# Kernel tuning notes

Hardware: AMD Instinct MI355X
Metric: run time of the kernel (lower is better)

## Reference

```python
import jax, jax.numpy as jnp
import numpy as np

N_NODES = 50000
N_EDGES = 800000
N_REL = 16
N_GRAPHS = 64
IN_DIM = 128
HID = 128
FC = 256
N_CLASSES = 16


def setup_inputs() -> dict:
    key = jax.random.key(0)
    ks = jax.random.split(key, 16)
    h = jax.random.normal(ks[0], (N_NODES, IN_DIM), dtype=jnp.float32)
    src = jax.random.randint(ks[1], (N_EDGES,), 0, N_NODES, dtype=jnp.int32)
    dst = jax.random.randint(ks[2], (N_EDGES,), 0, N_NODES, dtype=jnp.int32)
    rel_types = jax.random.randint(ks[3], (N_EDGES,), 0, N_REL, dtype=jnp.int32)
    graph_ids = jnp.sort(jax.random.randint(ks[4], (N_NODES,), 0, N_GRAPHS, dtype=jnp.int32))
    s1 = 1.0 / np.sqrt(IN_DIM)
    s2 = 1.0 / np.sqrt(HID)
    # RGCN layer 1: per-relation weights, self-loop weight, bias
    W1 = jax.random.normal(ks[5], (N_REL, IN_DIM, HID), dtype=jnp.float32) * s1
    Ws1 = jax.random.normal(ks[6], (IN_DIM, HID), dtype=jnp.float32) * s1
    b1 = jnp.zeros((HID,), dtype=jnp.float32)
    # RGCN layer 2
    W2 = jax.random.normal(ks[7], (N_REL, HID, HID), dtype=jnp.float32) * s2
    Ws2 = jax.random.normal(ks[8], (HID, HID), dtype=jnp.float32) * s2
    b2 = jnp.zeros((HID,), dtype=jnp.float32)
    # FC layer after mean pooling
    Wfc = jax.random.normal(ks[9], (HID, FC), dtype=jnp.float32) * s2
    bfc = jnp.zeros((FC,), dtype=jnp.float32)
    # classify head
    Wc = jax.random.normal(ks[10], (FC, N_CLASSES), dtype=jnp.float32) * (1.0 / np.sqrt(FC))
    bc = jnp.zeros((N_CLASSES,), dtype=jnp.float32)
    return dict(h=h, src=src, dst=dst, rel_types=rel_types, graph_ids=graph_ids,
                W1=W1, Ws1=Ws1, b1=b1, W2=W2, Ws2=Ws2, b2=b2,
                Wfc=Wfc, bfc=bfc, Wc=Wc, bc=bc)


def _rel_graph_conv(h, W, Ws, b, src, dst, rel):
    # dgl RelGraphConv (regularizer=None, self_loop=True, bias=True):
    # out[v] = sum_{e:(u->v)} W[rel_e] @ h[u] + Ws @ h[v] + b
    hW = jnp.einsum('ni,rio->rno', h, W)            # [R, N, out]
    msg = hW[rel, src]                               # [E, out] gather per edge
    agg = jax.ops.segment_sum(msg, dst, num_segments=N_NODES)
    return agg + h @ Ws + b


def _mean_nodes(h, graph_ids):
    sums = jax.ops.segment_sum(h, graph_ids, num_segments=N_GRAPHS)      # [G, D]
    cnts = jax.ops.segment_sum(jnp.ones((h.shape[0], 1), h.dtype), graph_ids,
                               num_segments=N_GRAPHS)                    # [G, 1]
    return sums / jnp.maximum(cnts, 1.0)


def reference(h, src, dst, rel_types, graph_ids,
              W1, Ws1, b1, W2, Ws2, b2, Wfc, bfc, Wc, bc):
    h = h.astype(jnp.float32)
    h = jax.nn.relu(_rel_graph_conv(h, W1, Ws1, b1, src, dst, rel_types))
    h = jax.nn.relu(_rel_graph_conv(h, W2, Ws2, b2, src, dst, rel_types))
    hg = _mean_nodes(h, graph_ids)                   # [G, HID]
    hg = jax.nn.relu(hg @ Wfc + bfc)                 # [G, FC]
    return jax.nn.softmax(hg @ Wc + bc, axis=1)      # [G, n_classes]
```

## Files before the change

kernel.cpp:

```cpp
#include <hip/hip_runtime.h>
#include <hip/hip_bf16.h>

#define N_NODES   50000
#define N_PAD     50048
#define N_EDGES   800000
#define N_REL     16
#define N_GRAPHS  64
#define DIM       128
#define FC_DIM    256
#define N_CLASSES 16

#define SB        50176
#define NBINS_P   (16 * SB)
#define NBLK_PP   784
#define NCOARSE   782
#define NCH       98
#define CHSZ      8192
#define POOL_CH   64
#define NBVIRT    13328
#define GRID_A    1024

#define NBLK_CX   27200
#define XW_TOTAL  (N_PAD * DIM + 2 * 17 * 16384)

#define WS_MARK   0
#define WS_HG     802816
#define WS_CNT    835584
#define WS_SRCOF  835840
#define MEMSET_SZ 4038912
#define WS_BLKH   4038912
#define WS_COFS   4345600
#define WS_PARTP  4348928
#define WS_BLKB   4352256
#define WS_RELB   4355584
#define WS_CIDMAP 4355840
#define WS_RTMP   7567104
#define WS_RECS   10767104
#define WS_OFFSD  13967104
#define WS_X1     14167552
#define WS_X2     26979840
#define WS_AGG    39792128
#define WS_WB     52604416
#define WS_T      53718528

typedef __attribute__((ext_vector_type(8))) short bf16x8;
typedef __attribute__((ext_vector_type(4))) float f32x4;

__device__ __forceinline__ void atomAddF(float* p, float v) {
#if defined(__gfx90a__) || defined(__gfx942__) || defined(__gfx950__)
    unsafeAtomicAdd(p, v);
#else
    atomicAdd(p, v);
#endif
}

__device__ __forceinline__ float bf2f(unsigned int u) {
    union { float f; unsigned int i; } x; x.i = u << 16; return x.f;
}
__device__ __forceinline__ unsigned short f2bf(float f) {
    union { float f; unsigned int u; } x; x.f = f;
    unsigned int r = x.u + 0x7fff + ((x.u >> 16) & 1);
    return (unsigned short)(r >> 16);
}
__device__ __forceinline__ void accum8(float* qa, uint4 u) {
    qa[0] += bf2f(u.x & 0xffff); qa[1] += bf2f(u.x >> 16);
    qa[2] += bf2f(u.y & 0xffff); qa[3] += bf2f(u.y >> 16);
    qa[4] += bf2f(u.z & 0xffff); qa[5] += bf2f(u.z >> 16);
    qa[6] += bf2f(u.w & 0xffff); qa[7] += bf2f(u.w >> 16);
}
__device__ __forceinline__ void pack16(const float* qa, unsigned short* dst) {
    #pragma unroll
    for (int j = 0; j < 2; ++j) {
        uint4 w;
        w.x = ((unsigned int)f2bf(qa[j*8+1]) << 16) | f2bf(qa[j*8+0]);
        w.y = ((unsigned int)f2bf(qa[j*8+3]) << 16) | f2bf(qa[j*8+2]);
        w.z = ((unsigned int)f2bf(qa[j*8+5]) << 16) | f2bf(qa[j*8+4]);
        w.w = ((unsigned int)f2bf(qa[j*8+7]) << 16) | f2bf(qa[j*8+6]);
        ((uint4*)dst)[j] = w;
    }
}

__global__ __launch_bounds__(256) void k_h1cx(
    const int* __restrict__ src, const int* __restrict__ dst, const int* __restrict__ rel,
    unsigned char* __restrict__ mark, int* __restrict__ blockHist,
    const float* __restrict__ h, unsigned short* __restrict__ x1,
    const float* __restrict__ W1, const float* __restrict__ Ws1,
    const float* __restrict__ W2, const float* __restrict__ Ws2,
    unsigned short* __restrict__ Wb)
{
    __shared__ int hl[NCOARSE];
    int t = threadIdx.x;
    if (blockIdx.x < NCH) {
        int b = blockIdx.x;
        for (int i = t; i < NCOARSE; i += 256) hl[i] = 0;
        __syncthreads();
        int e0 = b * CHSZ;
        int eend = min(e0 + CHSZ, N_EDGES);
        for (int e = e0 + t; e < eend; e += 256) {
            int d = dst[e];
            mark[rel[e] * SB + src[e]] = 1;
            atomicAdd(&hl[d >> 6], 1);
        }
        __syncthreads();
        for (int i = t; i < NCOARSE; i += 256) blockHist[b * NCOARSE + i] = hl[i];
    } else {
        int id = (blockIdx.x - NCH) * 256 + t;
        if (id < N_PAD * DIM) {
            int v = id >> 7;
            x1[id] = (v < N_NODES) ? f2bf(h[id]) : (unsigned short)0;
        } else {
            int tt = id - N_PAD * DIM;
            int l = tt / 278528, rem = tt % 278528;
            int r = rem >> 14, rr = rem & 16383;
            int n = rr >> 7, k = rr & 127;
            const float* W  = l ? W2 : W1;
            const float* Ws = l ? Ws2 : Ws1;
            float v = (r < 16) ? W[r * 16384 + k * 128 + n] : Ws[k * 128 + n];
            Wb[tt] = f2bf(v);
        }
    }
}

__global__ __launch_bounds__(256) void k_sA(
    const unsigned int* __restrict__ markU, int* __restrict__ partP,
    int* __restrict__ blockHist, int* __restrict__ cOffs)
{
    int t = threadIdx.x;
    if (blockIdx.x < NBLK_PP) {
        __shared__ int red[256];
        int b = blockIdx.x;
        unsigned int u = markU[b * 256 + t];
        red[t] = (int)((u & 1) + ((u >> 8) & 1) + ((u >> 16) & 1) + ((u >> 24) & 1));
        __syncthreads();
        for (int o = 128; o > 0; o >>= 1) {
            if (t < o) red[t] += red[t + o];
            __syncthreads();
        }
        if (t == 0) partP[b] = red[0];
    } else {
        __shared__ int sc[2][128];
        int i = blockIdx.x - NBLK_PP;
        int v = 0;
        if (t < NCH) v = blockHist[t * NCOARSE + i];
        if (t < 128) sc[0][t] = v;
        __syncthreads();
        int cur = 0, nxt = 1;
        #pragma unroll
        for (int o = 1; o < 128; o <<= 1) {
            if (t < 128) sc[nxt][t] = sc[cur][t] + ((t >= o) ? sc[cur][t - o] : 0);
            __syncthreads();
            int tmp = cur; cur = nxt; nxt = tmp;
        }
        if (t < NCH) blockHist[t * NCOARSE + i] = sc[cur][t] - v;
        if (t == NCH - 1) cOffs[i] = sc[cur][t];
    }
}

__global__ __launch_bounds__(1024) void k_sB(
    const int* __restrict__ partP, int* __restrict__ blkB, int* __restrict__ relB,
    int* __restrict__ cOffs)
{
    int t = threadIdx.x;
    if (blockIdx.x == 0) {
        __shared__ int s1[784], s2[784];
        __shared__ int tot[16], rbase[17];
        int rel = t / 49, pos = t - rel * 49;
        int v = (t < 784) ? partP[t] : 0;
        if (t < 784) s1[t] = v;
        __syncthreads();
        int* cur = s1; int* nxt = s2;
        for (int o = 1; o < 64; o <<= 1) {
            if (t < 784) nxt[t] = cur[t] + ((pos >= o) ? cur[t - o] : 0);
            __syncthreads();
            int* tmp = cur; cur = nxt; nxt = tmp;
        }
        if (t < 784 && pos == 48) tot[rel] = cur[t];
        __syncthreads();
        if (t == 0) {
            int base = 0;
            for (int r = 0; r < 16; ++r) { rbase[r] = base; base += (tot[r] + 63) & ~63; }
            rbase[16] = base;
        }
        __syncthreads();
        if (t < 784) blkB[t] = rbase[rel] + cur[t] - v;
        if (t < 17)  relB[t] = rbase[t];
    } else {
        __shared__ int c1[1024], c2[1024];
        int v = (t < NCOARSE) ? cOffs[t] : 0;
        c1[t] = v; __syncthreads();
        int* cur = c1; int* nxt = c2;
        for (int o = 1; o < 1024; o <<= 1) {
            nxt[t] = cur[t] + ((t >= o) ? cur[t - o] : 0);
            __syncthreads();
            int* tmp = cur; cur = nxt; nxt = tmp;
        }
        if (t < NCOARSE) cOffs[t] = cur[t] - v;
        if (t == NCOARSE) cOffs[NCOARSE] = cur[NCOARSE - 1];
    }
}

__global__ void k_scanPC(const unsigned int* __restrict__ markU, const int* __restrict__ blkB,
                         int* __restrict__ cidMap, int* __restrict__ srcOf) {
    __shared__ int s1[256], s2[256];
    int b = blockIdx.x, t = threadIdx.x;
    unsigned int u = markU[b * 256 + t];
    int f0 = (int)(u & 1), f1 = (int)((u >> 8) & 1);
    int f2 = (int)((u >> 16) & 1), f3 = (int)((u >> 24) & 1);
    int sum = f0 + f1 + f2 + f3;
    s1[t] = sum; __syncthreads();
    int* cur = s1; int* nxt = s2;
    for (int o = 1; o < 256; o <<= 1) {
        nxt[t] = cur[t] + ((t >= o) ? cur[t - o] : 0);
        __syncthreads();
        int* tmp = cur; cur = nxt; nxt = tmp;
    }
    int cid = blkB[b] + cur[t] - sum;
    int rel = b / 49;
    int key0 = b * 1024 + t * 4;
    int srcBase = key0 - rel * SB;
    if (f0) { cidMap[key0]     = cid; srcOf[cid] = srcBase;     cid++; }
    if (f1) { cidMap[key0 + 1] = cid; srcOf[cid] = srcBase + 1; cid++; }
    if (f2) { cidMap[key0 + 2] = cid; srcOf[cid] = srcBase + 2; cid++; }
    if (f3) { cidMap[key0 + 3] = cid; srcOf[cid] = srcBase + 3; cid++; }
}

__global__ __launch_bounds__(256) void k_scat1(
    const int* __restrict__ src, const int* __restrict__ dst, const int* __restrict__ rel,
    const int* __restrict__ cidMap, const int* __restrict__ blockHist,
    const int* __restrict__ cOffs, unsigned int* __restrict__ rtmp)
{
    __shared__ int baseL[NCOARSE];
    __shared__ int hl[NCOARSE];
    int b = blockIdx.x, t = threadIdx.x;
    for (int i = t; i < NCOARSE; i += 256) {
        baseL[i] = blockHist[b * NCOARSE + i] + cOffs[i];
        hl[i] = 0;
    }
    __syncthreads();
    int e0 = b * CHSZ;
    int eend = min(e0 + CHSZ, N_EDGES);
    for (int e = e0 + t; e < eend; e += 256) {
        int d = dst[e];
        int cid = cidMap[rel[e] * SB + src[e]];
        int c = d >> 6;
        int rank = atomicAdd(&hl[c], 1);
        rtmp[baseL[c] + rank] = ((unsigned int)cid << 6) | (unsigned int)(d & 63);
    }
}

__global__ __launch_bounds__(256) void k_p2(
    const unsigned int* __restrict__ rtmp, const int* __restrict__ coarseOffs,
    unsigned int* __restrict__ recs, int* __restrict__ offsD)
{
    __shared__ int cntL[64], exclL[65], cur2[64];
    int i = blockIdx.x, t = threadIdx.x;
    int segB = coarseOffs[i], segE = coarseOffs[i + 1];
    if (t < 64) { cntL[t] = 0; cur2[t] = 0; }
    __syncthreads();
    for (int e = segB + t; e < segE; e += 256)
        atomicAdd(&cntL[rtmp[e] & 63u], 1);
    __syncthreads();
    if (t == 0) {
        int run = segB;
        #pragma unroll
        for (int d = 0; d < 64; ++d) { exclL[d] = run; run += cntL[d]; }
        exclL[64] = run;
    }
    __syncthreads();
    if (t < 64) offsD[i * 64 + t] = exclL[t];
    if (t == 64) offsD[i * 64 + 64] = exclL[64];
    for (int e = segB + t; e < segE; e += 256) {
        unsigned int r = rtmp[e];
        int d = (int)(r & 63u);
        int rank = atomicAdd(&cur2[d], 1);
        recs[exclL[d] + rank] = r >> 6;
    }
}

__global__ __launch_bounds__(256) void k_phaseA(
    const unsigned short* __restrict__ x, const unsigned short* __restrict__ Wb,
    const int* __restrict__ srcOf, const int* __restrict__ relB,
    unsigned short* __restrict__ T)
{
    __shared__ __attribute__((aligned(16))) unsigned short Xs[64 * 136];
    __shared__ __attribute__((aligned(16))) unsigned short Cs[64 * 136];
    __shared__ int sRB[17];

    int tid = threadIdx.x;
    if (tid < 17) sRB[tid] = relB[tid];
    __syncthreads();
    int rtot = sRB[16];

    int row = tid >> 2, c0 = tid & 3;

    auto tileInfo = [&](int vb, int& trow0, int& tr) -> bool {
        int chunk = vb / 136;
        int lane = vb - chunk * 136;
        int r = lane >> 3;
        int i = chunk * 8 + (lane & 7);
        int base, cnt;
        if (r == 16) { base = rtot; cnt = N_PAD / 64; }
        else         { base = sRB[r]; cnt = (sRB[r + 1] - base) >> 6; }
        if (i >= cnt) return false;
        trow0 = base + i * 64; tr = r;
        return true;
    };

    int vb = blockIdx.x;
    int cur_row0, cur_r;
    while (vb < NBVIRT && !tileInfo(vb, cur_row0, cur_r)) vb += gridDim.x;
    if (vb >= NBVIRT) return;

    uint4 g0, g1, g2, g3;
    {
        int sr = (cur_r == 16) ? (cur_row0 - rtot + row) : srcOf[cur_row0 + row];
        const uint4* xp = (const uint4*)(x + (size_t)sr * DIM);
        g0 = xp[c0]; g1 = xp[c0 + 4]; g2 = xp[c0 + 8]; g3 = xp[c0 + 12];
    }

    int w = tid >> 6, l = tid & 63;
    int nl = l & 15, q = l >> 4;

    while (true) {
        {
            uint4* lp = (uint4*)(&Xs[row * 136]);
            lp[c0] = g0; lp[c0 + 4] = g1; lp[c0 + 8] = g2; lp[c0 + 12] = g3;
        }
        bf16x8 Bf[2][4];
        {
            const unsigned short* wr = Wb + cur_r * 16384;
            #pragma unroll
            for (int nt = 0; nt < 2; ++nt) {
                int n = w * 32 + nt * 16 + nl;
                #pragma unroll
                for (int kc = 0; kc < 4; ++kc)
                    Bf[nt][kc] = *(const bf16x8*)(wr + n * 128 + kc * 32 + q * 8);
            }
        }
        int nvb = vb + gridDim.x;
        int nxt_row0 = 0, nxt_r = 0;
        while (nvb < NBVIRT && !tileInfo(nvb, nxt_row0, nxt_r)) nvb += gridDim.x;
        bool nhave = (nvb < NBVIRT);
        if (nhave) {
            int sr = (nxt_r == 16) ? (nxt_row0 - rtot + row) : srcOf[nxt_row0 + row];
            const uint4* xp = (const uint4*)(x + (size_t)sr * DIM);
            g0 = xp[c0]; g1 = xp[c0 + 4]; g2 = xp[c0 + 8]; g3 = xp[c0 + 12];
        }
        __syncthreads();
        #pragma unroll
        for (int m = 0; m < 4; ++m) {
            f32x4 a0 = {0.f, 0.f, 0.f, 0.f}, a1 = {0.f, 0.f, 0.f, 0.f};
            #pragma unroll
            for (int kc = 0; kc < 4; ++kc) {
                bf16x8 a = *(const bf16x8*)(&Xs[(m * 16 + nl) * 136 + kc * 32 + q * 8]);
                a0 = __builtin_amdgcn_mfma_f32_16x16x32_bf16(a, Bf[0][kc], a0, 0, 0, 0);
                a1 = __builtin_amdgcn_mfma_f32_16x16x32_bf16(a, Bf[1][kc], a1, 0, 0, 0);
            }
            int colb = w * 32 + nl;
            #pragma unroll
            for (int reg = 0; reg < 4; ++reg) {
                int row2 = m * 16 + q * 4 + reg;
                int sw = ((row2 >> 3) & 1) << 4;
                Cs[row2 * 136 + (colb ^ sw)]        = f2bf(a0[reg]);
                Cs[row2 * 136 + ((colb + 16) ^ sw)] = f2bf(a1[reg]);
            }
        }
        __syncthreads();
        {
            unsigned short* Tb = T + (size_t)cur_row0 * DIM;
            #pragma unroll
            for (int it = 0; it < 4; ++it) {
                int c = tid + it * 256;
                int rw = c >> 4, k8 = c & 15;
                int sw = ((rw >> 3) & 1) << 4;
                uint4 vv = *(const uint4*)(&Cs[rw * 136 + ((k8 * 8) ^ sw)]);
                *(uint4*)(Tb + rw * DIM + k8 * 8) = vv;
            }
        }
        if (!nhave) break;
        vb = nvb; cur_row0 = nxt_row0; cur_r = nxt_r;
    }
}

__global__ __launch_bounds__(256) void k_phaseB(
    const unsigned short* __restrict__ T, const unsigned int* __restrict__ recs,
    const int* __restrict__ offsD, const int* __restrict__ relB,
    const float* __restrict__ bias,
    unsigned short* __restrict__ aggOut, int relu)
{
    __shared__ int sOffs[33];
    __shared__ float sBias[128];
    __shared__ int sSelf;
    int tid = threadIdx.x;
    int v0 = blockIdx.x * 32;
    if (tid < 33) sOffs[tid] = offsD[v0 + tid];
    if (tid == 40) sSelf = relB[16];
    if (tid >= 64 && tid < 96) ((float4*)sBias)[tid - 64] = ((const float4*)bias)[tid - 64];
    __syncthreads();

    int g = tid >> 3, s = tid & 7;
    int dst = v0 + g;
    float qa[16];
    #pragma unroll
    for (int i = 0; i < 16; ++i) qa[i] = sBias[s * 16 + i];

    int beg = sOffs[g], end = sOffs[g + 1];
    int e = beg;
    for (; e + 3 < end; e += 4) {
        unsigned int c0 = recs[e], c1 = recs[e+1], c2 = recs[e+2], c3 = recs[e+3];
        const uint4* t0 = (const uint4*)(T + (size_t)c0 * DIM + s * 16);
        const uint4* t1 = (const uint4*)(T + (size_t)c1 * DIM + s * 16);
        const uint4* t2 = (const uint4*)(T + (size_t)c2 * DIM + s * 16);
        const uint4* t3 = (const uint4*)(T + (size_t)c3 * DIM + s * 16);
        uint4 a0 = t0[0], a1 = t0[1], b0 = t1[0], b1 = t1[1];
        uint4 cc0 = t2[0], cc1 = t2[1], d0 = t3[0], d1 = t3[1];
        accum8(qa, a0); accum8(qa + 8, a1);
        accum8(qa, b0); accum8(qa + 8, b1);
        accum8(qa, cc0); accum8(qa + 8, cc1);
        accum8(qa, d0); accum8(qa + 8, d1);
    }
    for (; e < end; ++e) {
        unsigned int c = recs[e];
        const uint4* tp = (const uint4*)(T + (size_t)c * DIM + s * 16);
        uint4 u0 = tp[0], u1 = tp[1];
        accum8(qa, u0); accum8(qa + 8, u1);
    }
    {
        const uint4* tp = (const uint4*)(T + (size_t)(sSelf + dst) * DIM + s * 16);
        uint4 u0 = tp[0], u1 = tp[1];
        accum8(qa, u0); accum8(qa + 8, u1);
    }

    if (relu) {
        #pragma unroll
        for (int i = 0; i < 16; ++i) qa[i] = fmaxf(qa[i], 0.f);
    }
    pack16(qa, aggOut + (size_t)dst * DIM + s * 16);
}

__global__ void k_pool(const unsigned short* __restrict__ agg2, const int* __restrict__ gids,
                       float* __restrict__ hg_sum, int* __restrict__ cnt)
{
    int d  = threadIdx.x;
    int n0 = blockIdx.x * POOL_CH;
    int nend = min(n0 + POOL_CH, N_NODES);
    if (n0 >= N_NODES) return;
    int curg = gids[n0];
    float run = 0.f;
    for (int n = n0; n < nend; ++n) {
        int g = gids[n];
        if (g != curg) { atomAddF(&hg_sum[curg*DIM + d], run); run = 0.f; curg = g; }
        run += fmaxf(bf2f((unsigned int)agg2[n*DIM + d]), 0.f);
    }
    atomAddF(&hg_sum[curg*DIM + d], run);
    if (d == 0) {
        int cg = gids[n0]; int rl = 0;
        for (int n = n0; n < nend; ++n) {
            int g = gids[n];
            if (g != cg) { atomicAdd(&cnt[cg], rl); rl = 0; cg = g; }
            rl++;
        }
        atomicAdd(&cnt[cg], rl);
    }
}

__global__ __launch_bounds__(256) void k_head(
    const float* __restrict__ hg_sum, const int* __restrict__ cnt,
    const float* __restrict__ Wfc, const float* __restrict__ bfc,
    const float* __restrict__ Wc, const float* __restrict__ bc,
    float* __restrict__ out)
{
    int g = blockIdx.x, t = threadIdx.x;
    __shared__ float hgl[DIM];
    __shared__ float fcl[FC_DIM];
    __shared__ float lg[N_CLASSES];
    if (t < DIM) {
        float c = (float)max(cnt[g], 1);
        hgl[t] = hg_sum[g*DIM + t] / c;
    }
    __syncthreads();
    {
        float sv = bfc[t];
        #pragma unroll 4
        for (int k = 0; k < DIM; ++k) sv += hgl[k] * Wfc[k*FC_DIM + t];
        fcl[t] = fmaxf(sv, 0.f);
    }
    __syncthreads();
    if (t < N_CLASSES) {
        float lgt = bc[t];
        #pragma unroll 4
        for (int k = 0; k < FC_DIM; ++k) lgt += fcl[k] * Wc[k*N_CLASSES + t];
        lg[t] = lgt;
    }
    __syncthreads();
    if (t < N_CLASSES) {
        float m = lg[0];
        #pragma unroll
        for (int c = 1; c < N_CLASSES; ++c) m = fmaxf(m, lg[c]);
        float sden = 0.f;
        #pragma unroll
        for (int c = 0; c < N_CLASSES; ++c) sden += expf(lg[c] - m);
        out[g*N_CLASSES + t] = expf(lg[t] - m) / sden;
    }
}

extern "C" void kernel_launch(void* const* d_in, const int* in_sizes, int n_in,
                              void* d_out, int out_size, void* d_ws, size_t ws_size,
                              hipStream_t stream)
{
    const float* h   = (const float*)d_in[0];
    const int*   src = (const int*)d_in[1];
    const int*   dst = (const int*)d_in[2];
    const int*   rel = (const int*)d_in[3];
    const int*   gid = (const int*)d_in[4];
    const float* W1  = (const float*)d_in[5];
    const float* Ws1 = (const float*)d_in[6];
    const float* b1  = (const float*)d_in[7];
    const float* W2  = (const float*)d_in[8];
    const float* Ws2 = (const float*)d_in[9];
    const float* b2  = (const float*)d_in[10];
    const float* Wfc = (const float*)d_in[11];
    const float* bfc = (const float*)d_in[12];
    const float* Wc  = (const float*)d_in[13];
    const float* bc  = (const float*)d_in[14];
    float* out = (float*)d_out;

    char* ws = (char*)d_ws;
    unsigned char* mark = (unsigned char*)(ws + WS_MARK);
    float* hgsum = (float*)(ws + WS_HG);
    int*   cnt   = (int*)(ws + WS_CNT);
    int*   srcOf = (int*)(ws + WS_SRCOF);
    int*   blkH  = (int*)(ws + WS_BLKH);
    int*   cOffs = (int*)(ws + WS_COFS);
    int*   partP = (int*)(ws + WS_PARTP);
    int*   blkB  = (int*)(ws + WS_BLKB);
    int*   relB  = (int*)(ws + WS_RELB);
    int*   cidMap= (int*)(ws + WS_CIDMAP);
    unsigned int* rtmp = (unsigned int*)(ws + WS_RTMP);
    unsigned int* recs = (unsigned int*)(ws + WS_RECS);
    int*   offsD = (int*)(ws + WS_OFFSD);
    unsigned short* x1  = (unsigned short*)(ws + WS_X1);
    unsigned short* x2  = (unsigned short*)(ws + WS_X2);
    unsigned short* agg = (unsigned short*)(ws + WS_AGG);
    unsigned short* Wb  = (unsigned short*)(ws + WS_WB);
    unsigned short* T   = (unsigned short*)(ws + WS_T);

    hipMemsetAsync(mark, 0, MEMSET_SZ, stream);

    k_h1cx<<<NCH + NBLK_CX, 256, 0, stream>>>(src, dst, rel, mark, blkH,
                                              h, x1, W1, Ws1, W2, Ws2, Wb);
    k_sA<<<NBLK_PP + NCOARSE, 256, 0, stream>>>((const unsigned int*)mark, partP,
                                                blkH, cOffs);
    k_sB<<<2, 1024, 0, stream>>>(partP, blkB, relB, cOffs);
    k_scanPC<<<NBLK_PP, 256, 0, stream>>>((const unsigned int*)mark, blkB, cidMap, srcOf);

    k_scat1<<<NCH, 256, 0, stream>>>(src, dst, rel, cidMap, blkH, cOffs, rtmp);
    k_p2<<<NCOARSE, 256, 0, stream>>>(rtmp, cOffs, recs, offsD);

    k_phaseA<<<GRID_A, 256, 0, stream>>>(x1, Wb, srcOf, relB, T);
    k_phaseB<<<N_PAD / 32, 256, 0, stream>>>(T, recs, offsD, relB, b1, x2, 1);
    k_phaseA<<<GRID_A, 256, 0, stream>>>(x2, Wb + 17 * 16384, srcOf, relB, T);
    k_phaseB<<<N_PAD / 32, 256, 0, stream>>>(T, recs, offsD, relB, b2, agg, 0);

    k_pool<<<(N_PAD + POOL_CH - 1) / POOL_CH, 128, 0, stream>>>(agg, gid, hgsum, cnt);
    k_head<<<N_GRAPHS, 256, 0, stream>>>(hgsum, cnt, Wfc, bfc, Wc, bc, out);
}
```

Baseline: 408.5 us.

## Fuse mean-pool into second aggregation kernel and increase edge-binning chunk count

The second aggregation kernel now applies ReLU and reduces its 32-node tile per graph in shared memory, then atomically adds into the graph sums. This removes the bf16 write and re-read of the final node features and one kernel launch. Node counts per graph are now found by binary search on the sorted graph ids in the head kernel, so the separate count atomics go away. The edge-binning chunk count is also quadrupled with smaller chunks, and the coarse scan is widened to handle 392 chunks. That gives more parallel blocks in the histogram and scatter steps, at the cost of a larger block histogram.

```diff
diff --git a/kernel.cpp b/kernel.cpp
--- a/kernel.cpp
+++ b/kernel.cpp
@@ -14,9 +14,8 @@
 #define NBINS_P   (16 * SB)
 #define NBLK_PP   784
 #define NCOARSE   782
-#define NCH       98
-#define CHSZ      8192
-#define POOL_CH   64
+#define NCH       392
+#define CHSZ      2048
 #define NBVIRT    13328
 #define GRID_A    1024
 
@@ -29,19 +28,18 @@
 #define WS_SRCOF  835840
 #define MEMSET_SZ 4038912
 #define WS_BLKH   4038912
-#define WS_COFS   4345600
-#define WS_PARTP  4348928
-#define WS_BLKB   4352256
-#define WS_RELB   4355584
-#define WS_CIDMAP 4355840
-#define WS_RTMP   7567104
-#define WS_RECS   10767104
-#define WS_OFFSD  13967104
-#define WS_X1     14167552
-#define WS_X2     26979840
-#define WS_AGG    39792128
-#define WS_WB     52604416
-#define WS_T      53718528
+#define WS_COFS   5265152
+#define WS_PARTP  5268480
+#define WS_BLKB   5271808
+#define WS_RELB   5275136
+#define WS_CIDMAP 5275392
+#define WS_RTMP   8486656
+#define WS_RECS   11686656
+#define WS_OFFSD  14886656
+#define WS_X1     15087104
+#define WS_X2     27899392
+#define WS_WB     40711680
+#define WS_T      41825792
 
 typedef __attribute__((ext_vector_type(8))) short bf16x8;
 typedef __attribute__((ext_vector_type(4))) float f32x4;
@@ -138,21 +136,23 @@
         }
         if (t == 0) partP[b] = red[0];
     } else {
-        __shared__ int sc[2][128];
+        __shared__ int sc[2][256];
         int i = blockIdx.x - NBLK_PP;
-        int v = 0;
-        if (t < NCH) v = blockHist[t * NCOARSE + i];
-        if (t < 128) sc[0][t] = v;
-        __syncthreads();
-        int cur = 0, nxt = 1;
-        #pragma unroll
-        for (int o = 1; o < 128; o <<= 1) {
-            if (t < 128) sc[nxt][t] = sc[cur][t] + ((t >= o) ? sc[cur][t - o] : 0);
+        int j0 = 2 * t, j1 = 2 * t + 1;
+        int v0 = (j0 < NCH) ? blockHist[j0 * NCOARSE + i] : 0;
+        int v1 = (j1 < NCH) ? blockHist[j1 * NCOARSE + i] : 0;
+        int p = v0 + v1;
+        sc[0][t] = p; __syncthreads();
+        int cur = 0;
+        for (int o = 1; o < 256; o <<= 1) {
+            sc[cur ^ 1][t] = sc[cur][t] + ((t >= o) ? sc[cur][t - o] : 0);
             __syncthreads();
-            int tmp = cur; cur = nxt; nxt = tmp;
-        }
-        if (t < NCH) blockHist[t * NCOARSE + i] = sc[cur][t] - v;
-        if (t == NCH - 1) cOffs[i] = sc[cur][t];
+            cur ^= 1;
+        }
+        int excl = sc[cur][t] - p;
+        if (j0 < NCH) blockHist[j0 * NCOARSE + i] = excl;
+        if (j1 < NCH) blockHist[j1 * NCOARSE + i] = excl + v0;
+        if (t == 255) cOffs[i] = sc[cur][255];
     }
 }
 
@@ -386,16 +386,20 @@
     const unsigned short* __restrict__ T, const unsigned int* __restrict__ recs,
     const int* __restrict__ offsD, const int* __restrict__ relB,
     const float* __restrict__ bias,
-    unsigned short* __restrict__ aggOut, int relu)
+    unsigned short* __restrict__ aggOut,
+    const int* __restrict__ gids, float* __restrict__ hg_sum, int pool)
 {
     __shared__ int sOffs[33];
     __shared__ float sBias[128];
     __shared__ int sSelf;
+    __shared__ float Sp[32][129];
+    __shared__ int sGid[32];
     int tid = threadIdx.x;
     int v0 = blockIdx.x * 32;
     if (tid < 33) sOffs[tid] = offsD[v0 + tid];
     if (tid == 40) sSelf = relB[16];
     if (tid >= 64 && tid < 96) ((float4*)sBias)[tid - 64] = ((const float4*)bias)[tid - 64];
+    if (pool && tid < 32) sGid[tid] = (v0 + tid < N_NODES) ? gids[v0 + tid] : -1;
     __syncthreads();
 
     int g = tid >> 3, s = tid & 7;
@@ -431,41 +435,30 @@
         accum8(qa, u0); accum8(qa + 8, u1);
     }
 
-    if (relu) {
+    if (!pool) {
         #pragma unroll
         for (int i = 0; i < 16; ++i) qa[i] = fmaxf(qa[i], 0.f);
-    }
-    pack16(qa, aggOut + (size_t)dst * DIM + s * 16);
-}
-
-__global__ void k_pool(const unsigned short* __restrict__ agg2, const int* __restrict__ gids,
-                       float* __restrict__ hg_sum, int* __restrict__ cnt)
-{
-    int d  = threadIdx.x;
-    int n0 = blockIdx.x * POOL_CH;
-    int nend = min(n0 + POOL_CH, N_NODES);
-    if (n0 >= N_NODES) return;
-    int curg = gids[n0];
-    float run = 0.f;
-    for (int n = n0; n < nend; ++n) {
-        int g = gids[n];
-        if (g != curg) { atomAddF(&hg_sum[curg*DIM + d], run); run = 0.f; curg = g; }
-        run += fmaxf(bf2f((unsigned int)agg2[n*DIM + d]), 0.f);
-    }
-    atomAddF(&hg_sum[curg*DIM + d], run);
-    if (d == 0) {
-        int cg = gids[n0]; int rl = 0;
-        for (int n = n0; n < nend; ++n) {
-            int g = gids[n];
-            if (g != cg) { atomicAdd(&cnt[cg], rl); rl = 0; cg = g; }
-            rl++;
-        }
-        atomicAdd(&cnt[cg], rl);
+        pack16(qa, aggOut + (size_t)dst * DIM + s * 16);
+    } else {
+        #pragma unroll
+        for (int i = 0; i < 16; ++i) Sp[g][s * 16 + i] = fmaxf(qa[i], 0.f);
+        __syncthreads();
+        int d = tid & 127, hh = tid >> 7;
+        float run = 0.f; int curg = -2;
+        for (int n = hh * 16; n < hh * 16 + 16; ++n) {
+            int g2 = sGid[n];
+            if (g2 != curg) {
+                if (curg >= 0) atomAddF(&hg_sum[curg * DIM + d], run);
+                run = 0.f; curg = g2;
+            }
+            run += Sp[n][d];
+        }
+        if (curg >= 0) atomAddF(&hg_sum[curg * DIM + d], run);
     }
 }
 
 __global__ __launch_bounds__(256) void k_head(
-    const float* __restrict__ hg_sum, const int* __restrict__ cnt,
+    const float* __restrict__ hg_sum, const int* __restrict__ gids,
     const float* __restrict__ Wfc, const float* __restrict__ bfc,
     const float* __restrict__ Wc, const float* __restrict__ bc,
     float* __restrict__ out)
@@ -474,8 +467,18 @@
     __shared__ float hgl[DIM];
     __shared__ float fcl[FC_DIM];
     __shared__ float lg[N_CLASSES];
+    __shared__ int scnt;
+    if (t == 0) {
+        int lo = 0, hi = N_NODES;
+        while (lo < hi) { int mid = (lo + hi) >> 1; if (gids[mid] < g) lo = mid + 1; else hi = mid; }
+        int lb = lo;
+        hi = N_NODES;
+        while (lo < hi) { int mid = (lo + hi) >> 1; if (gids[mid] <= g) lo = mid + 1; else hi = mid; }
+        scnt = lo - lb;
+    }
+    __syncthreads();
     if (t < DIM) {
-        float c = (float)max(cnt[g], 1);
+        float c = (float)max(scnt, 1);
         hgl[t] = hg_sum[g*DIM + t] / c;
     }
     __syncthreads();
@@ -528,7 +531,6 @@
     char* ws = (char*)d_ws;
     unsigned char* mark = (unsigned char*)(ws + WS_MARK);
     float* hgsum = (float*)(ws + WS_HG);
-    int*   cnt   = (int*)(ws + WS_CNT);
     int*   srcOf = (int*)(ws + WS_SRCOF);
     int*   blkH  = (int*)(ws + WS_BLKH);
     int*   cOffs = (int*)(ws + WS_COFS);
@@ -541,7 +543,6 @@
     int*   offsD = (int*)(ws + WS_OFFSD);
     unsigned short* x1  = (unsigned short*)(ws + WS_X1);
     unsigned short* x2  = (unsigned short*)(ws + WS_X2);
-    unsigned short* agg = (unsigned short*)(ws + WS_AGG);
     unsigned short* Wb  = (unsigned short*)(ws + WS_WB);
     unsigned short* T   = (unsigned short*)(ws + WS_T);
 
@@ -558,10 +559,9 @@
     k_p2<<<NCOARSE, 256, 0, stream>>>(rtmp, cOffs, recs, offsD);
 
     k_phaseA<<<GRID_A, 256, 0, stream>>>(x1, Wb, srcOf, relB, T);
-    k_phaseB<<<N_PAD / 32, 256, 0, stream>>>(T, recs, offsD, relB, b1, x2, 1);
+    k_phaseB<<<N_PAD / 32, 256, 0, stream>>>(T, recs, offsD, relB, b1, x2, gid, hgsum, 0);
     k_phaseA<<<GRID_A, 256, 0, stream>>>(x2, Wb + 17 * 16384, srcOf, relB, T);
-    k_phaseB<<<N_PAD / 32, 256, 0, stream>>>(T, recs, offsD, relB, b2, agg, 0);
-
-    k_pool<<<(N_PAD + POOL_CH - 1) / POOL_CH, 128, 0, stream>>>(agg, gid, hgsum, cnt);
-    k_head<<<N_GRAPHS, 256, 0, stream>>>(hgsum, cnt, Wfc, bfc, Wc, bc, out);
-}
+    k_phaseB<<<N_PAD / 32, 256, 0, stream>>>(T, recs, offsD, relB, b2, x2, gid, hgsum, 1);
+
+    k_head<<<N_GRAPHS, 256, 0, stream>>>(hgsum, gid, Wfc, bfc, Wc, bc, out);
+}
```

New measurement: 377.0 us. -7.7%, faster.
